# Kernel tuning notes

Measured on AMD Instinct MI355X. Metric: run time of the kernel, lower is better.

The kernel has to match this reference:

```python
import jax, jax.numpy as jnp
import numpy as np
from jax import lax

GRAVITY = 9.8
DT = 0.1
MAX_STEPS = 200


def _conv(x, w, b):
    # x: [N,C,H,W], w: [O,I,3,3] (PyTorch OIHW), padding=1 -> SAME
    y = lax.conv_general_dilated(x, w, window_strides=(1, 1), padding='SAME',
                                 dimension_numbers=('NCHW', 'OIHW', 'NCHW'))
    return y + b[None, :, None, None]


def _maxpool2(x):
    return lax.reduce_window(x, -jnp.inf, lax.max,
                             window_dimensions=(1, 1, 2, 2),
                             window_strides=(1, 1, 2, 2), padding='VALID')


def setup_inputs() -> dict:
    key = jax.random.key(0)
    ks = jax.random.split(key, 12)
    B = 256
    x = jax.random.normal(ks[0], (B, 12, 128, 128), dtype=jnp.float32)

    def he(k, shape, fan_in):
        return jax.random.normal(k, shape, dtype=jnp.float32) * np.float32(np.sqrt(2.0 / fan_in))

    w1 = he(ks[1], (32, 12, 3, 3), 12 * 9); b1 = jnp.zeros((32,), jnp.float32)
    w2 = he(ks[2], (64, 32, 3, 3), 32 * 9); b2 = jnp.zeros((64,), jnp.float32)
    w3 = he(ks[3], (64, 64, 3, 3), 64 * 9); b3 = jnp.zeros((64,), jnp.float32)
    w4 = he(ks[4], (64, 64, 3, 3), 64 * 9); b4 = jnp.zeros((64,), jnp.float32)
    wl1 = he(ks[5], (128, 64 * 8 * 8), 64 * 8 * 8); bl1 = jnp.zeros((128,), jnp.float32)
    wl2 = he(ks[6], (4, 128), 128); bl2 = jnp.zeros((4,), jnp.float32)
    return {'x': x, 'w1': w1, 'b1': b1, 'w2': w2, 'b2': b2, 'w3': w3, 'b3': b3,
            'w4': w4, 'b4': b4, 'wl1': wl1, 'bl1': bl1, 'wl2': wl2, 'bl2': bl2}


def _forward(x, w1, b1, w2, b2, w3, b3, w4, b4, wl1, bl1, wl2, bl2):
    h = _maxpool2(jax.nn.relu(_conv(x, w1, b1)))   # [B,32,64,64]
    h = _maxpool2(jax.nn.relu(_conv(h, w2, b2)))   # [B,64,32,32]
    h = _maxpool2(jax.nn.relu(_conv(h, w3, b3)))   # [B,64,16,16]
    h = _maxpool2(jax.nn.relu(_conv(h, w4, b4)))   # [B,64,8,8]
    h = h.reshape(h.shape[0], -1)                  # [B,4096]
    h = jax.nn.relu(h @ wl1.T + bl1)               # [B,128]
    state = h @ wl2.T + bl2                        # [B,4]

    px, py, vx, vy = state[:, 0], state[:, 1], state[:, 2], state[:, 3]

    def step(carry, _):
        cx, cy, cvy = carry
        nvy = cvy - GRAVITY * DT
        nx = cx + vx * DT
        ny = jnp.maximum(cy + nvy * DT, 0.0)
        return (nx, ny, nvy), None

    (fx, _, _), _ = lax.scan(step, (px, py, vy), None, length=MAX_STEPS)
    return fx


def reference(x, w1, b1, w2, b2, w3, b3, w4, b4, wl1, bl1, wl2, bl2):
    return _forward(x, w1, b1, w2, b2, w3, b3, w4, b4, wl1, bl1, wl2, bl2)
```

## Files before the change

kernel.cpp:

```cpp
#include <hip/hip_runtime.h>


typedef _Float16 f16;
typedef _Float16 f16x8 __attribute__((ext_vector_type(8)));
typedef _Float16 f16x4 __attribute__((ext_vector_type(4)));
typedef float f32x4 __attribute__((ext_vector_type(4)));
typedef float f32x16 __attribute__((ext_vector_type(16)));

__global__ __launch_bounds__(512)
void pack_weights(const float* __restrict__ w1, const float* __restrict__ w2,
                  const float* __restrict__ w3, const float* __restrict__ w4,
                  f16* __restrict__ apack) {
  int idx = blockIdx.x * 512 + threadIdx.x;
  int frag = idx >> 9;
  int e = idx & 511;
  int lane = e >> 3, j = e & 7;
  float v = 0.f;
  if (frag < 9) {
    int kh = frag / 3, kw = frag % 3;
    int oc = lane & 31;
    int ic = (lane >> 5) * 8 + j;
    if (ic < 12) v = w1[((oc * 12 + ic) * 3 + kh) * 3 + kw];
  } else if (frag < 45) {
    int f = frag - 9;
    int ocg = f & 1;
    int sk = f >> 1;
    int ks = sk & 1, sh = sk >> 1;
    int kh = sh / 3, kw = sh % 3;
    int oc = ocg * 32 + (lane & 31);
    int ic = ks * 16 + (lane >> 5) * 8 + j;
    v = w2[((oc * 32 + ic) * 3 + kh) * 3 + kw];
  } else if (frag < 117) {
    int f = frag - 45;
    int ocg = f & 1;
    int sk = f >> 1;
    int ks = sk & 3, sh = sk >> 2;
    int kh = sh / 3, kw = sh % 3;
    int oc = ocg * 32 + (lane & 31);
    int ic = ks * 16 + (lane >> 5) * 8 + j;
    v = w3[((oc * 64 + ic) * 3 + kh) * 3 + kw];
  } else {
    int f = frag - 117;
    int sk = f >> 2, og = f & 3;
    int sh = sk >> 1, ks = sk & 1;
    int kh = sh / 3, kw = sh % 3;
    int row16 = lane & 15, kg = lane >> 4;
    int oc = og * 16 + row16;
    int ic = ks * 32 + kg * 8 + j;
    v = w4[((oc * 64 + ic) * 3 + kh) * 3 + kw];
  }
  apack[idx] = (f16)v;
}

__global__ __launch_bounds__(256)
void pack_wl1(const float* __restrict__ wl1, f16* __restrict__ wl1h) {
  int i = (blockIdx.x * 256 + threadIdx.x) * 4;
  float4 v = *(const float4*)(wl1 + i);
  f16x4 h = { (f16)v.x, (f16)v.y, (f16)v.z, (f16)v.w };
  *(f16x4*)(wl1h + i) = h;
}

__global__ __launch_bounds__(512)
void conv1_mfma(const float* __restrict__ x, const f16* __restrict__ apack,
                const float* __restrict__ bias, f16* __restrict__ hout) {
  constexpr int W = 128, H = 128;
  constexpr int PADB = 48, ROWB = 130 * PADB;
  constexpr int TPB = 8;
  __shared__ char smem[6 * ROWB];
  const int tid = threadIdx.x;
  const int n = blockIdx.y;
  const int R0 = blockIdx.x * (TPB * 4);

  if (tid < 36) {
    int slot = tid / 6, r = tid % 6;
    int px = (r >= 3) ? 129 : 0;
    int ch = r % 3;
    *(float4*)(smem + slot * ROWB + px * PADB + ch * 16) =
        make_float4(0.f, 0.f, 0.f, 0.f);
  }

  const int g = tid >> 4;
  const int l16 = tid & 15;
  const int Q = l16 >> 2, q = l16 & 3;

  auto load_row = [&](int ri) -> float4 {
    float4 v = make_float4(0.f, 0.f, 0.f, 0.f);
    if (l16 < 12 && ri >= 0 && ri < H)
      v = *(const float4*)(x + ((size_t)(n * 12 + l16) * H + ri) * W + g * 4);
    return v;
  };
  auto xpose_write = [&](float4 av, int slot) {
    float4 t1, t2;
    {
      float sx = __shfl_xor(av.x, 1), sy = __shfl_xor(av.y, 1);
      float sz = __shfl_xor(av.z, 1), sw = __shfl_xor(av.w, 1);
      bool odd = q & 1;
      t1.x = odd ? sy : av.x;  t1.y = odd ? av.y : sx;
      t1.z = odd ? sw : av.z;  t1.w = odd ? av.w : sz;
    }
    {
      float sx = __shfl_xor(t1.x, 2), sy = __shfl_xor(t1.y, 2);
      float sz = __shfl_xor(t1.z, 2), sw = __shfl_xor(t1.w, 2);
      bool hi2 = q & 2;
      t2.x = hi2 ? sz : t1.x;  t2.y = hi2 ? sw : t1.y;
      t2.z = hi2 ? t1.z : sx;  t2.w = hi2 ? t1.w : sy;
    }
    f16x4 h = { (f16)t2.x, (f16)t2.y, (f16)t2.z, (f16)t2.w };
    *(f16x4*)(smem + slot * ROWB + (g * 4 + q + 1) * PADB + Q * 8) = h;
  };

  const int wv = tid >> 6, l = tid & 63;
  const int rp = wv >> 2;
  const int pxb = (wv & 3) * 32;
  const int rl0 = rp * 2;
  const int ln = l & 31;
  const int hi = l >> 5;

  f16x8 A[9];
#pragma unroll
  for (int ks = 0; ks < 9; ++ks)
    A[ks] = *(const f16x8*)(apack + ((ks << 9) + (l << 3)));

  float4 a[6];
#pragma unroll
  for (int i = 0; i < 6; ++i) a[i] = load_row(R0 - 1 + i);
#pragma unroll
  for (int i = 0; i < 6; ++i) xpose_write(a[i], i);
  __syncthreads();

  int s0 = 0;
  for (int t = 0; t < TPB; ++t) {
    if (t + 1 < TPB) {
#pragma unroll
      for (int i = 0; i < 4; ++i) a[i] = load_row(R0 + 4 * t + 5 + i);
    }
    f32x16 acc0 = (f32x16)0.f, acc1 = (f32x16)0.f;
#pragma unroll
    for (int kw = 0; kw < 3; ++kw) {
      const char* bcol = smem + (pxb + ln + kw) * PADB + hi * 16;
      f16x8 R[4];
#pragma unroll
      for (int j = 0; j < 4; ++j) {
        int sl = s0 + rl0 + j; if (sl >= 6) sl -= 6;
        R[j] = *(const f16x8*)(bcol + sl * ROWB);
      }
#pragma unroll
      for (int kh = 0; kh < 3; ++kh) {
        acc0 = __builtin_amdgcn_mfma_f32_32x32x16_f16(A[kh * 3 + kw], R[kh],     acc0, 0, 0, 0);
        acc1 = __builtin_amdgcn_mfma_f32_32x32x16_f16(A[kh * 3 + kw], R[kh + 1], acc1, 0, 0, 0);
      }
    }
    {
      const int pr = (R0 >> 1) + 2 * t + rp;
#pragma unroll
      for (int gg = 0; gg < 4; ++gg) {
        float v[4];
#pragma unroll
        for (int c = 0; c < 4; ++c) {
          float m = fmaxf(acc0[gg * 4 + c], acc1[gg * 4 + c]);
          v[c] = fmaxf(m, __shfl_xor(m, 1));
        }
        if ((l & 1) == 0) {
          const int pw = (pxb + ln) >> 1;
          const int oc0 = gg * 8 + hi * 4;
          f16x4 pk;
#pragma unroll
          for (int c = 0; c < 4; ++c)
            pk[c] = (f16)fmaxf(v[c] + bias[oc0 + c], 0.f);
          *(f16x4*)(hout + (((size_t)(n * 64 + pr) * 64 + pw) * 32 + oc0)) = pk;
        }
      }
    }
    __syncthreads();
    if (t + 1 < TPB) {
#pragma unroll
      for (int i = 0; i < 4; ++i) {
        int sl = s0 + i; if (sl >= 6) sl -= 6;
        xpose_write(a[i], sl);
      }
      __syncthreads();
    }
    s0 += 4; if (s0 >= 6) s0 -= 6;
  }
}

__global__ __launch_bounds__(256)
void conv2_roll(const f16* __restrict__ hin, const f16* __restrict__ apack,
                const float* __restrict__ bias, f16* __restrict__ hout) {
  constexpr int C = 32, W = 64, H = 64;
  constexpr int PADB = 80, ROWB = 66 * PADB;
  constexpr int TPB = 4;
  __shared__ char smem[6 * ROWB];
  const int tid = threadIdx.x;
  const int n = blockIdx.y;
  const int R0 = blockIdx.x * (TPB * 4);

  auto chunk_ld = [&](int c, int rbase) -> float4 {
    int rowl = c / 264, rem = c - rowl * 264;
    int px = rem >> 2, kc = rem & 3;
    int ri = rbase + rowl, gx = px - 1;
    float4 v = make_float4(0.f, 0.f, 0.f, 0.f);
    if (ri >= 0 && ri < H && gx >= 0 && gx < W)
      v = *(const float4*)(hin + (((size_t)(n * H + ri) * W + gx) * C + kc * 8));
    return v;
  };
  auto chunk_st = [&](int c, int sbase, float4 v) {
    int rowl = c / 264, rem = c - rowl * 264;
    int px = rem >> 2, kc = rem & 3;
    int slot = sbase + rowl; if (slot >= 6) slot -= 6;
    *(float4*)(smem + slot * ROWB + px * PADB + kc * 16) = v;
  };

  {
    float4 a[7];
#pragma unroll
    for (int it = 0; it < 7; ++it) {
      int c = tid + it * 256;
      a[it] = (c < 1584) ? chunk_ld(c, R0 - 1) : make_float4(0.f, 0.f, 0.f, 0.f);
    }
#pragma unroll
    for (int it = 0; it < 7; ++it) {
      int c = tid + it * 256;
      if (c < 1584) chunk_st(c, 0, a[it]);
    }
  }
  __syncthreads();

  const int wv = tid >> 6, l = tid & 63;
  const int rp = wv >> 1;
  const int pxb = (wv & 1) * 32;
  const int rl0 = rp * 2;
  const int ln = l & 31;
  const int hi = l >> 5;

  float4 a[5];
  int s04 = 0;
  for (int t = 0; t < TPB; ++t) {
    if (t + 1 < TPB) {
#pragma unroll
      for (int it = 0; it < 5; ++it) {
        int c = tid + it * 256;
        a[it] = (c < 1056) ? chunk_ld(c, R0 + 4 * t + 5)
                           : make_float4(0.f, 0.f, 0.f, 0.f);
      }
    }
    f32x16 acc[2][2];
    acc[0][0] = (f32x16)0.f; acc[0][1] = (f32x16)0.f;
    acc[1][0] = (f32x16)0.f; acc[1][1] = (f32x16)0.f;
#pragma unroll
    for (int sh = 0; sh < 9; ++sh) {
      const int kh = sh / 3, kw = sh % 3;
      f16x8 A[2][2];
#pragma unroll
      for (int ks = 0; ks < 2; ++ks)
#pragma unroll
        for (int ocg = 0; ocg < 2; ++ocg)
          A[ks][ocg] = *(const f16x8*)(apack + ((((sh * 2 + ks) * 2 + ocg) << 9) + (l << 3)));
#pragma unroll
      for (int rowi = 0; rowi < 2; ++rowi) {
        int sl = s04 + rl0 + rowi + kh; if (sl >= 6) sl -= 6;
        const char* base = smem + sl * ROWB + (pxb + ln + kw) * PADB + hi * 16;
#pragma unroll
        for (int ks = 0; ks < 2; ++ks) {
          f16x8 B = *(const f16x8*)(base + ks * 32);
          acc[rowi][0] = __builtin_amdgcn_mfma_f32_32x32x16_f16(A[ks][0], B, acc[rowi][0], 0, 0, 0);
          acc[rowi][1] = __builtin_amdgcn_mfma_f32_32x32x16_f16(A[ks][1], B, acc[rowi][1], 0, 0, 0);
        }
      }
    }
    {
      const int pr = (R0 >> 1) + 2 * t + rp;
#pragma unroll
      for (int ocg = 0; ocg < 2; ++ocg) {
#pragma unroll
        for (int gg = 0; gg < 4; ++gg) {
          float v[4];
#pragma unroll
          for (int c = 0; c < 4; ++c) {
            float m = fmaxf(acc[0][ocg][gg * 4 + c], acc[1][ocg][gg * 4 + c]);
            v[c] = fmaxf(m, __shfl_xor(m, 1));
          }
          if ((l & 1) == 0) {
            const int pw = (pxb + ln) >> 1;
            const int oc0 = ocg * 32 + gg * 8 + hi * 4;
            f16x4 pk;
#pragma unroll
            for (int c = 0; c < 4; ++c)
              pk[c] = (f16)fmaxf(v[c] + bias[oc0 + c], 0.f);
            *(f16x4*)(hout + (((size_t)(n * 32 + pr) * 32 + pw) * 64 + oc0)) = pk;
          }
        }
      }
    }
    __syncthreads();
    if (t + 1 < TPB) {
#pragma unroll
      for (int it = 0; it < 5; ++it) {
        int c = tid + it * 256;
        if (c < 1056) chunk_st(c, s04, a[it]);
      }
      __syncthreads();
    }
    s04 += 4; if (s04 >= 6) s04 -= 6;
  }
}

template<int C, int W, int H, int BR, int PADB>
__global__ __launch_bounds__(256)
void conv_shift32(const f16* __restrict__ hin, const f16* __restrict__ apack,
                  const float* __restrict__ bias, f16* __restrict__ hout) {
  constexpr int KS16 = C / 16;
  constexpr int SR = BR + 2;
  constexpr int ROWB = (W + 2) * PADB;
  __shared__ char smem[SR * ROWB];
  const int tid = threadIdx.x;
  const int n = blockIdx.y;
  const int r0 = blockIdx.x * BR;
  constexpr int CPC = C / 8;
  constexpr int TOTC = SR * (W + 2) * CPC;
  constexpr int NITER = (TOTC + 255) / 256;
  {
    float4 stg[NITER];
#pragma unroll
    for (int it = 0; it < NITER; ++it) {
      const int t = tid + it * 256;
      float4 v = make_float4(0.f, 0.f, 0.f, 0.f);
      if (t < TOTC) {
        int sr = t / ((W + 2) * CPC);
        int rem = t - sr * ((W + 2) * CPC);
        int px = rem / CPC;
        int kc = rem - px * CPC;
        int ri = r0 + sr - 1;
        int gx = px - 1;
        if (ri >= 0 && ri < H && gx >= 0 && gx < W)
          v = *(const float4*)(hin + (((size_t)(n * H + ri) * W + gx) * C + kc * 8));
      }
      stg[it] = v;
    }
#pragma unroll
    for (int it = 0; it < NITER; ++it) {
      const int t = tid + it * 256;
      if (t < TOTC) {
        int sr = t / ((W + 2) * CPC);
        int rem = t - sr * ((W + 2) * CPC);
        int px = rem / CPC;
        int kc = rem - px * CPC;
        *(float4*)(smem + sr * ROWB + px * PADB + kc * 16) = stg[it];
      }
    }
  }
  __syncthreads();

  const int wv = tid >> 6, l = tid & 63;
  constexpr int WPP = W / 32;
  const int rp = wv / WPP;
  const int pxb = (wv % WPP) * 32;
  const int rl0 = rp * 2;
  const int ln = l & 31;
  const int hi = l >> 5;
  const int px0 = pxb + ln;

  f32x16 acc[2][2];
  acc[0][0] = (f32x16)0.f; acc[0][1] = (f32x16)0.f;
  acc[1][0] = (f32x16)0.f; acc[1][1] = (f32x16)0.f;

#pragma unroll
  for (int sh = 0; sh < 9; ++sh) {
    const int kh = sh / 3, kw = sh % 3;
    f16x8 A[KS16][2];
#pragma unroll
    for (int ks = 0; ks < KS16; ++ks)
#pragma unroll
      for (int ocg = 0; ocg < 2; ++ocg)
        A[ks][ocg] = *(const f16x8*)(apack + ((((sh * KS16 + ks) * 2 + ocg) << 9) + (l << 3)));
#pragma unroll
    for (int rowi = 0; rowi < 2; ++rowi) {
      const char* base = smem + (rl0 + rowi + kh) * ROWB + (px0 + kw) * PADB + hi * 16;
#pragma unroll
      for (int ks = 0; ks < KS16; ++ks) {
        f16x8 B = *(const f16x8*)(base + ks * 32);
        acc[rowi][0] = __builtin_amdgcn_mfma_f32_32x32x16_f16(A[ks][0], B, acc[rowi][0], 0, 0, 0);
        acc[rowi][1] = __builtin_amdgcn_mfma_f32_32x32x16_f16(A[ks][1], B, acc[rowi][1], 0, 0, 0);
      }
    }
  }
  constexpr int PH = H / 2, PW = W / 2;
  const int pr = blockIdx.x * (BR / 2) + rp;
#pragma unroll
  for (int ocg = 0; ocg < 2; ++ocg) {
#pragma unroll
    for (int gg = 0; gg < 4; ++gg) {
      float v[4];
#pragma unroll
      for (int c = 0; c < 4; ++c) {
        float m = fmaxf(acc[0][ocg][gg * 4 + c], acc[1][ocg][gg * 4 + c]);
        v[c] = fmaxf(m, __shfl_xor(m, 1));
      }
      if ((l & 1) == 0) {
        const int pw = (pxb + ln) >> 1;
        const int oc0 = ocg * 32 + gg * 8 + hi * 4;
        f16x4 pk;
#pragma unroll
        for (int c = 0; c < 4; ++c)
          pk[c] = (f16)fmaxf(v[c] + bias[oc0 + c], 0.f);
        *(f16x4*)(hout + (((size_t)(n * PH + pr) * PW + pw) * 64 + oc0)) = pk;
      }
    }
  }
}

template<int C, int W, int H, int BR, int KS, int PADB, int PGn, bool NCHW_OUT>
__global__ __launch_bounds__(256)
void conv_shift(const f16* __restrict__ hin, const f16* __restrict__ apack,
                const float* __restrict__ bias, void* __restrict__ hout) {
  constexpr int SR = BR + 2;
  constexpr int ROWB = (W + 2) * PADB;
  __shared__ char smem[SR * ROWB];
  const int tid = threadIdx.x;
  const int n = blockIdx.y;
  const int r0 = blockIdx.x * BR;
  constexpr int CPC = C / 8;
  constexpr int TOTC = SR * (W + 2) * CPC;
  constexpr int NITER = (TOTC + 255) / 256;
  {
    float4 stg[NITER];
#pragma unroll
    for (int it = 0; it < NITER; ++it) {
      const int t = tid + it * 256;
      float4 v = make_float4(0.f, 0.f, 0.f, 0.f);
      if (t < TOTC) {
        int sr = t / ((W + 2) * CPC);
        int rem = t - sr * ((W + 2) * CPC);
        int px = rem / CPC;
        int kc = rem - px * CPC;
        int ri = r0 + sr - 1;
        int gx = px - 1;
        if (ri >= 0 && ri < H && gx >= 0 && gx < W)
          v = *(const float4*)(hin + (((size_t)(n * H + ri) * W + gx) * C + kc * 8));
      }
      stg[it] = v;
    }
#pragma unroll
    for (int it = 0; it < NITER; ++it) {
      const int t = tid + it * 256;
      if (t < TOTC) {
        int sr = t / ((W + 2) * CPC);
        int rem = t - sr * ((W + 2) * CPC);
        int px = rem / CPC;
        int kc = rem - px * CPC;
        *(float4*)(smem + sr * ROWB + px * PADB + kc * 16) = stg[it];
      }
    }
  }
  __syncthreads();

  const int wv = tid >> 6, l = tid & 63;
  constexpr int WPP = W / (16 * PGn);
  const int rp = wv / WPP;
  const int pxb = (wv % WPP) * 16 * PGn;
  const int rl0 = rp * 2;
  const int lp = l & 15, kg = l >> 4;
  const int px0 = pxb + lp;

  f32x4 acc[2][PGn][4];
#pragma unroll
  for (int a = 0; a < 2; ++a)
#pragma unroll
    for (int b = 0; b < PGn; ++b)
#pragma unroll
      for (int c = 0; c < 4; ++c)
        acc[a][b][c] = (f32x4){0.f, 0.f, 0.f, 0.f};

#pragma unroll
  for (int sh = 0; sh < 9; ++sh) {
    const int kh = sh / 3, kw = sh % 3;
    f16x8 A[KS][4];
#pragma unroll
    for (int ks = 0; ks < KS; ++ks)
#pragma unroll
      for (int og = 0; og < 4; ++og)
        A[ks][og] = *(const f16x8*)(apack + ((((sh * KS + ks) * 4 + og) << 9) + (l << 3)));
#pragma unroll
    for (int rowi = 0; rowi < 2; ++rowi) {
      const char* base = smem + (rl0 + rowi + kh) * ROWB;
#pragma unroll
      for (int pg = 0; pg < PGn; ++pg) {
#pragma unroll
        for (int ks = 0; ks < KS; ++ks) {
          f16x8 B = *(const f16x8*)(base + (px0 + pg * 16 + kw) * PADB + ks * 64 + kg * 16);
#pragma unroll
          for (int og = 0; og < 4; ++og)
            acc[rowi][pg][og] =
                __builtin_amdgcn_mfma_f32_16x16x32_f16(A[ks][og], B, acc[rowi][pg][og], 0, 0, 0);
        }
      }
    }
  }
  constexpr int PH = H / 2, PW = W / 2;
  const int pr = blockIdx.x * (BR / 2) + rp;
#pragma unroll
  for (int pg = 0; pg < PGn; ++pg) {
#pragma unroll
    for (int og = 0; og < 4; ++og) {
      float v[4];
#pragma unroll
      for (int c = 0; c < 4; ++c) {
        float m = fmaxf(acc[0][pg][og][c], acc[1][pg][og][c]);
        v[c] = fmaxf(m, __shfl_xor(m, 1));
      }
      if ((l & 1) == 0) {
        const int pw = (pxb + pg * 16 + lp) >> 1;
        const int oc0 = og * 16 + kg * 4;
        if constexpr (NCHW_OUT) {
          float* o = (float*)hout;
#pragma unroll
          for (int c = 0; c < 4; ++c)
            o[(((size_t)n * 64 + oc0 + c) * PH + pr) * PW + pw] =
                fmaxf(v[c] + bias[oc0 + c], 0.f);
        } else {
          f16x4 pk;
#pragma unroll
          for (int c = 0; c < 4; ++c)
            pk[c] = (f16)fmaxf(v[c] + bias[oc0 + c], 0.f);
          *(f16x4*)((f16*)hout + (((size_t)(n * PH + pr) * PW + pw) * 64 + oc0)) = pk;
        }
      }
    }
  }
}

__global__ __launch_bounds__(1024)
void fc_head(const float* __restrict__ h4, const f16* __restrict__ wl1h,
             const float* __restrict__ bl1, const float* __restrict__ wl2,
             const float* __restrict__ bl2, float* __restrict__ out) {
  __shared__ float rows[2][4096];
  __shared__ float red[8 * 128 * 2];
  __shared__ float red2[2 * 128];
  const int tid = threadIdx.x;
  const int b0 = blockIdx.x * 2;
  {
    const float4* src = (const float4*)(h4 + (size_t)b0 * 4096);
    float4* dst = (float4*)rows;
    for (int t = tid; t < 2048; t += 1024) dst[t] = src[t];
  }
  __syncthreads();

  const int nn = tid & 127;
  const int ks = tid >> 7;
  const f16x8* wp = (const f16x8*)(wl1h + (size_t)nn * 4096 + ks * 512);
  const float4* x0 = (const float4*)(&rows[0][ks * 512]);
  const float4* x1 = (const float4*)(&rows[1][ks * 512]);
  float s0 = 0.f, s1 = 0.f;
#pragma unroll 4
  for (int i = 0; i < 64; ++i) {
    f16x8 w8 = wp[i];
    float4 a0 = x0[2 * i], a1 = x0[2 * i + 1];
    float4 b0 = x1[2 * i], b1 = x1[2 * i + 1];
    float w0 = (float)w8[0], w1 = (float)w8[1], w2 = (float)w8[2], w3 = (float)w8[3];
    float w4 = (float)w8[4], w5 = (float)w8[5], w6 = (float)w8[6], w7 = (float)w8[7];
    s0 = fmaf(w0, a0.x, fmaf(w1, a0.y, fmaf(w2, a0.z, fmaf(w3, a0.w, s0))));
    s0 = fmaf(w4, a1.x, fmaf(w5, a1.y, fmaf(w6, a1.z, fmaf(w7, a1.w, s0))));
    s1 = fmaf(w0, b0.x, fmaf(w1, b0.y, fmaf(w2, b0.z, fmaf(w3, b0.w, s1))));
    s1 = fmaf(w4, b1.x, fmaf(w5, b1.y, fmaf(w6, b1.z, fmaf(w7, b1.w, s1))));
  }
  red[(ks * 128 + nn) * 2 + 0] = s0;
  red[(ks * 128 + nn) * 2 + 1] = s1;
  __syncthreads();

  if (tid < 256) {
    const int r = tid >> 7, n2 = tid & 127;
    float h = bl1[n2];
#pragma unroll
    for (int k = 0; k < 8; ++k) h += red[(k * 128 + n2) * 2 + r];
    h = fmaxf(h, 0.f);
    red2[r * 128 + n2] = h * (wl2[n2] + 20.0f * wl2[256 + n2]);
  }
  __syncthreads();
#pragma unroll
  for (int s = 64; s > 0; s >>= 1) {
    if (tid < 2 * s) {
      int r = tid / s, i = tid - r * s;
      red2[r * 128 + i] += red2[r * 128 + i + s];
    }
    __syncthreads();
  }
  if (tid < 2) out[b0 + tid] = red2[tid * 128] + bl2[0] + 20.0f * bl2[2];
}

extern "C" void kernel_launch(void* const* d_in, const int* in_sizes, int n_in,
                              void* d_out, int out_size, void* d_ws, size_t ws_size,
                              hipStream_t stream) {
  const float* x   = (const float*)d_in[0];
  const float* w1  = (const float*)d_in[1];
  const float* b1  = (const float*)d_in[2];
  const float* w2  = (const float*)d_in[3];
  const float* b2  = (const float*)d_in[4];
  const float* w3  = (const float*)d_in[5];
  const float* b3  = (const float*)d_in[6];
  const float* w4  = (const float*)d_in[7];
  const float* b4  = (const float*)d_in[8];
  const float* wl1 = (const float*)d_in[9];
  const float* bl1 = (const float*)d_in[10];
  const float* wl2 = (const float*)d_in[11];
  const float* bl2 = (const float*)d_in[12];
  float* out = (float*)d_out;
  char* ws = (char*)d_ws;

  f16* apack = (f16*)ws;
  f16* wl1h  = (f16*)(ws + 524288u);
  f16* h1 = (f16*)(ws + 2097152u);
  f16* h2 = (f16*)(ws + 69206016u);
  f16* h3 = (f16*)(ws + 102760448u);
  float* h4 = (float*)(ws + 111149056u);

  pack_weights<<<189, 512, 0, stream>>>(w1, w2, w3, w4, apack);
  pack_wl1<<<512, 256, 0, stream>>>(wl1, wl1h);
  conv1_mfma<<<dim3(4, 256), 512, 0, stream>>>(x, apack, b1, h1);
  conv2_roll<<<dim3(4, 256), 256, 0, stream>>>(h1, apack + 9 * 512, b2, h2);
  conv_shift32<64, 32, 32, 8, 144><<<dim3(4, 256), 256, 0, stream>>>(
      h2, apack + 45 * 512, b3, h3);
  conv_shift<64, 16, 16, 8, 2, 144, 1, true><<<dim3(2, 256), 256, 0, stream>>>(
      h3, apack + 117 * 512, b4, (void*)h4);
  fc_head<<<128, 1024, 0, stream>>>(h4, wl1h, bl1, wl2, bl2, out);
}
```

Baseline: 233.3 us.

## Fuse conv4, pooling and FC head into one kernel; merge weight packing

Conv4 with its pool and the FC head are merged into one kernel with one block per sample. The block keeps the pooled 64x8x8 activation in shared memory and runs the FC dot products directly from it, which removes the h4 round-trip through global memory and one launch. The two weight-packing kernels are also merged into one launch. In exchange each sample gets a single block of 512 threads, and every block reads the full fp16 wl1 matrix (1 MB), where before each block served two samples.

```diff
diff --git a/kernel.cpp b/kernel.cpp
--- a/kernel.cpp
+++ b/kernel.cpp
@@ -8,9 +8,17 @@
 typedef float f32x16 __attribute__((ext_vector_type(16)));
 
 __global__ __launch_bounds__(512)
-void pack_weights(const float* __restrict__ w1, const float* __restrict__ w2,
-                  const float* __restrict__ w3, const float* __restrict__ w4,
-                  f16* __restrict__ apack) {
+void pack_all(const float* __restrict__ w1, const float* __restrict__ w2,
+              const float* __restrict__ w3, const float* __restrict__ w4,
+              const float* __restrict__ wl1, f16* __restrict__ apack,
+              f16* __restrict__ wl1h) {
+  if (blockIdx.x >= 189) {
+    int i = ((blockIdx.x - 189) * 512 + threadIdx.x) * 4;
+    float4 v = *(const float4*)(wl1 + i);
+    f16x4 h = { (f16)v.x, (f16)v.y, (f16)v.z, (f16)v.w };
+    *(f16x4*)(wl1h + i) = h;
+    return;
+  }
   int idx = blockIdx.x * 512 + threadIdx.x;
   int frag = idx >> 9;
   int e = idx & 511;
@@ -52,14 +60,6 @@
   apack[idx] = (f16)v;
 }
 
-__global__ __launch_bounds__(256)
-void pack_wl1(const float* __restrict__ wl1, f16* __restrict__ wl1h) {
-  int i = (blockIdx.x * 256 + threadIdx.x) * 4;
-  float4 v = *(const float4*)(wl1 + i);
-  f16x4 h = { (f16)v.x, (f16)v.y, (f16)v.z, (f16)v.w };
-  *(f16x4*)(wl1h + i) = h;
-}
-
 __global__ __launch_bounds__(512)
 void conv1_mfma(const float* __restrict__ x, const f16* __restrict__ apack,
                 const float* __restrict__ bias, f16* __restrict__ hout) {
@@ -409,43 +409,44 @@
   }
 }
 
-template<int C, int W, int H, int BR, int KS, int PADB, int PGn, bool NCHW_OUT>
-__global__ __launch_bounds__(256)
-void conv_shift(const f16* __restrict__ hin, const f16* __restrict__ apack,
-                const float* __restrict__ bias, void* __restrict__ hout) {
-  constexpr int SR = BR + 2;
-  constexpr int ROWB = (W + 2) * PADB;
-  __shared__ char smem[SR * ROWB];
+__global__ __launch_bounds__(512)
+void tail_fused(const f16* __restrict__ hin, const f16* __restrict__ apack4,
+                const float* __restrict__ bias, const f16* __restrict__ wl1h,
+                const float* __restrict__ bl1, const float* __restrict__ wl2,
+                const float* __restrict__ bl2, float* __restrict__ out) {
+  constexpr int C = 64, W = 16, H = 16;
+  constexpr int PADB = 144, ROWB = 18 * PADB;
+  __shared__ char smem[18 * ROWB];
+  __shared__ float hbuf[4096];
+  __shared__ float red[4 * 128];
+  __shared__ float red2[128];
   const int tid = threadIdx.x;
-  const int n = blockIdx.y;
-  const int r0 = blockIdx.x * BR;
-  constexpr int CPC = C / 8;
-  constexpr int TOTC = SR * (W + 2) * CPC;
-  constexpr int NITER = (TOTC + 255) / 256;
+  const int n = blockIdx.x;
+
+  constexpr int CPC = 8, TOTC = 18 * 18 * CPC;
   {
-    float4 stg[NITER];
-#pragma unroll
-    for (int it = 0; it < NITER; ++it) {
-      const int t = tid + it * 256;
+    float4 stg[6];
+#pragma unroll
+    for (int it = 0; it < 6; ++it) {
+      const int t = tid + it * 512;
       float4 v = make_float4(0.f, 0.f, 0.f, 0.f);
       if (t < TOTC) {
-        int sr = t / ((W + 2) * CPC);
-        int rem = t - sr * ((W + 2) * CPC);
+        int sr = t / (18 * CPC);
+        int rem = t - sr * (18 * CPC);
         int px = rem / CPC;
         int kc = rem - px * CPC;
-        int ri = r0 + sr - 1;
-        int gx = px - 1;
+        int ri = sr - 1, gx = px - 1;
         if (ri >= 0 && ri < H && gx >= 0 && gx < W)
           v = *(const float4*)(hin + (((size_t)(n * H + ri) * W + gx) * C + kc * 8));
       }
       stg[it] = v;
     }
 #pragma unroll
-    for (int it = 0; it < NITER; ++it) {
-      const int t = tid + it * 256;
+    for (int it = 0; it < 6; ++it) {
+      const int t = tid + it * 512;
       if (t < TOTC) {
-        int sr = t / ((W + 2) * CPC);
-        int rem = t - sr * ((W + 2) * CPC);
+        int sr = t / (18 * CPC);
+        int rem = t - sr * (18 * CPC);
         int px = rem / CPC;
         int kc = rem - px * CPC;
         *(float4*)(smem + sr * ROWB + px * PADB + kc * 16) = stg[it];
@@ -454,137 +455,88 @@
   }
   __syncthreads();
 
-  const int wv = tid >> 6, l = tid & 63;
-  constexpr int WPP = W / (16 * PGn);
-  const int rp = wv / WPP;
-  const int pxb = (wv % WPP) * 16 * PGn;
-  const int rl0 = rp * 2;
-  const int lp = l & 15, kg = l >> 4;
-  const int px0 = pxb + lp;
-
-  f32x4 acc[2][PGn][4];
-#pragma unroll
-  for (int a = 0; a < 2; ++a)
-#pragma unroll
-    for (int b = 0; b < PGn; ++b)
-#pragma unroll
-      for (int c = 0; c < 4; ++c)
-        acc[a][b][c] = (f32x4){0.f, 0.f, 0.f, 0.f};
-
-#pragma unroll
-  for (int sh = 0; sh < 9; ++sh) {
-    const int kh = sh / 3, kw = sh % 3;
-    f16x8 A[KS][4];
-#pragma unroll
-    for (int ks = 0; ks < KS; ++ks)
-#pragma unroll
-      for (int og = 0; og < 4; ++og)
-        A[ks][og] = *(const f16x8*)(apack + ((((sh * KS + ks) * 4 + og) << 9) + (l << 3)));
-#pragma unroll
-    for (int rowi = 0; rowi < 2; ++rowi) {
-      const char* base = smem + (rl0 + rowi + kh) * ROWB;
-#pragma unroll
-      for (int pg = 0; pg < PGn; ++pg) {
-#pragma unroll
-        for (int ks = 0; ks < KS; ++ks) {
-          f16x8 B = *(const f16x8*)(base + (px0 + pg * 16 + kw) * PADB + ks * 64 + kg * 16);
+  {
+    const int wv = tid >> 6, l = tid & 63;
+    const int lp = l & 15, kg = l >> 4;
+    const int rl0 = wv * 2;
+
+    f32x4 acc[2][4];
+#pragma unroll
+    for (int a = 0; a < 2; ++a)
+#pragma unroll
+      for (int o = 0; o < 4; ++o) acc[a][o] = (f32x4){0.f, 0.f, 0.f, 0.f};
+
+#pragma unroll
+    for (int sh = 0; sh < 9; ++sh) {
+      const int kh = sh / 3, kw = sh % 3;
+      f16x8 A[2][4];
+#pragma unroll
+      for (int ks = 0; ks < 2; ++ks)
+#pragma unroll
+        for (int og = 0; og < 4; ++og)
+          A[ks][og] = *(const f16x8*)(apack4 + ((((sh * 2 + ks) * 4 + og) << 9) + (l << 3)));
+#pragma unroll
+      for (int rowi = 0; rowi < 2; ++rowi) {
+        const char* base = smem + (rl0 + rowi + kh) * ROWB;
+#pragma unroll
+        for (int ks = 0; ks < 2; ++ks) {
+          f16x8 B = *(const f16x8*)(base + (lp + kw) * PADB + ks * 64 + kg * 16);
 #pragma unroll
           for (int og = 0; og < 4; ++og)
-            acc[rowi][pg][og] =
-                __builtin_amdgcn_mfma_f32_16x16x32_f16(A[ks][og], B, acc[rowi][pg][og], 0, 0, 0);
+            acc[rowi][og] =
+                __builtin_amdgcn_mfma_f32_16x16x32_f16(A[ks][og], B, acc[rowi][og], 0, 0, 0);
         }
       }
     }
-  }
-  constexpr int PH = H / 2, PW = W / 2;
-  const int pr = blockIdx.x * (BR / 2) + rp;
-#pragma unroll
-  for (int pg = 0; pg < PGn; ++pg) {
 #pragma unroll
     for (int og = 0; og < 4; ++og) {
       float v[4];
 #pragma unroll
       for (int c = 0; c < 4; ++c) {
-        float m = fmaxf(acc[0][pg][og][c], acc[1][pg][og][c]);
+        float m = fmaxf(acc[0][og][c], acc[1][og][c]);
         v[c] = fmaxf(m, __shfl_xor(m, 1));
       }
       if ((l & 1) == 0) {
-        const int pw = (pxb + pg * 16 + lp) >> 1;
+        const int pw = lp >> 1;
         const int oc0 = og * 16 + kg * 4;
-        if constexpr (NCHW_OUT) {
-          float* o = (float*)hout;
-#pragma unroll
-          for (int c = 0; c < 4; ++c)
-            o[(((size_t)n * 64 + oc0 + c) * PH + pr) * PW + pw] =
-                fmaxf(v[c] + bias[oc0 + c], 0.f);
-        } else {
-          f16x4 pk;
-#pragma unroll
-          for (int c = 0; c < 4; ++c)
-            pk[c] = (f16)fmaxf(v[c] + bias[oc0 + c], 0.f);
-          *(f16x4*)((f16*)hout + (((size_t)(n * PH + pr) * PW + pw) * 64 + oc0)) = pk;
-        }
-      }
-    }
-  }
-}
-
-__global__ __launch_bounds__(1024)
-void fc_head(const float* __restrict__ h4, const f16* __restrict__ wl1h,
-             const float* __restrict__ bl1, const float* __restrict__ wl2,
-             const float* __restrict__ bl2, float* __restrict__ out) {
-  __shared__ float rows[2][4096];
-  __shared__ float red[8 * 128 * 2];
-  __shared__ float red2[2 * 128];
-  const int tid = threadIdx.x;
-  const int b0 = blockIdx.x * 2;
+#pragma unroll
+        for (int c = 0; c < 4; ++c)
+          hbuf[(oc0 + c) * 64 + wv * 8 + pw] = fmaxf(v[c] + bias[oc0 + c], 0.f);
+      }
+    }
+  }
+  __syncthreads();
+
   {
-    const float4* src = (const float4*)(h4 + (size_t)b0 * 4096);
-    float4* dst = (float4*)rows;
-    for (int t = tid; t < 2048; t += 1024) dst[t] = src[t];
-  }
-  __syncthreads();
-
-  const int nn = tid & 127;
-  const int ks = tid >> 7;
-  const f16x8* wp = (const f16x8*)(wl1h + (size_t)nn * 4096 + ks * 512);
-  const float4* x0 = (const float4*)(&rows[0][ks * 512]);
-  const float4* x1 = (const float4*)(&rows[1][ks * 512]);
-  float s0 = 0.f, s1 = 0.f;
+    const int nn = tid & 127;
+    const int ks = tid >> 7;
+    const f16x8* wp = (const f16x8*)(wl1h + (size_t)nn * 4096 + ks * 1024);
+    const float4* xr = (const float4*)(&hbuf[ks * 1024]);
+    float s = 0.f;
 #pragma unroll 4
-  for (int i = 0; i < 64; ++i) {
-    f16x8 w8 = wp[i];
-    float4 a0 = x0[2 * i], a1 = x0[2 * i + 1];
-    float4 b0 = x1[2 * i], b1 = x1[2 * i + 1];
-    float w0 = (float)w8[0], w1 = (float)w8[1], w2 = (float)w8[2], w3 = (float)w8[3];
-    float w4 = (float)w8[4], w5 = (float)w8[5], w6 = (float)w8[6], w7 = (float)w8[7];
-    s0 = fmaf(w0, a0.x, fmaf(w1, a0.y, fmaf(w2, a0.z, fmaf(w3, a0.w, s0))));
-    s0 = fmaf(w4, a1.x, fmaf(w5, a1.y, fmaf(w6, a1.z, fmaf(w7, a1.w, s0))));
-    s1 = fmaf(w0, b0.x, fmaf(w1, b0.y, fmaf(w2, b0.z, fmaf(w3, b0.w, s1))));
-    s1 = fmaf(w4, b1.x, fmaf(w5, b1.y, fmaf(w6, b1.z, fmaf(w7, b1.w, s1))));
-  }
-  red[(ks * 128 + nn) * 2 + 0] = s0;
-  red[(ks * 128 + nn) * 2 + 1] = s1;
-  __syncthreads();
-
-  if (tid < 256) {
-    const int r = tid >> 7, n2 = tid & 127;
-    float h = bl1[n2];
-#pragma unroll
-    for (int k = 0; k < 8; ++k) h += red[(k * 128 + n2) * 2 + r];
+    for (int i = 0; i < 128; ++i) {
+      f16x8 w8 = wp[i];
+      float4 a0 = xr[2 * i], a1 = xr[2 * i + 1];
+      s = fmaf((float)w8[0], a0.x, fmaf((float)w8[1], a0.y,
+          fmaf((float)w8[2], a0.z, fmaf((float)w8[3], a0.w, s))));
+      s = fmaf((float)w8[4], a1.x, fmaf((float)w8[5], a1.y,
+          fmaf((float)w8[6], a1.z, fmaf((float)w8[7], a1.w, s))));
+    }
+    red[ks * 128 + nn] = s;
+  }
+  __syncthreads();
+  if (tid < 128) {
+    float h = bl1[tid] + red[tid] + red[128 + tid] + red[256 + tid] + red[384 + tid];
     h = fmaxf(h, 0.f);
-    red2[r * 128 + n2] = h * (wl2[n2] + 20.0f * wl2[256 + n2]);
+    red2[tid] = h * (wl2[tid] + 20.0f * wl2[256 + tid]);
   }
   __syncthreads();
 #pragma unroll
   for (int s = 64; s > 0; s >>= 1) {
-    if (tid < 2 * s) {
-      int r = tid / s, i = tid - r * s;
-      red2[r * 128 + i] += red2[r * 128 + i + s];
-    }
+    if (tid < s) red2[tid] += red2[tid + s];
     __syncthreads();
   }
-  if (tid < 2) out[b0 + tid] = red2[tid * 128] + bl2[0] + 20.0f * bl2[2];
+  if (tid == 0) out[n] = red2[0] + bl2[0] + 20.0f * bl2[2];
 }
 
 extern "C" void kernel_launch(void* const* d_in, const int* in_sizes, int n_in,
@@ -611,15 +563,12 @@
   f16* h1 = (f16*)(ws + 2097152u);
   f16* h2 = (f16*)(ws + 69206016u);
   f16* h3 = (f16*)(ws + 102760448u);
-  float* h4 = (float*)(ws + 111149056u);
-
-  pack_weights<<<189, 512, 0, stream>>>(w1, w2, w3, w4, apack);
-  pack_wl1<<<512, 256, 0, stream>>>(wl1, wl1h);
+
+  pack_all<<<445, 512, 0, stream>>>(w1, w2, w3, w4, wl1, apack, wl1h);
   conv1_mfma<<<dim3(4, 256), 512, 0, stream>>>(x, apack, b1, h1);
   conv2_roll<<<dim3(4, 256), 256, 0, stream>>>(h1, apack + 9 * 512, b2, h2);
   conv_shift32<64, 32, 32, 8, 144><<<dim3(4, 256), 256, 0, stream>>>(
       h2, apack + 45 * 512, b3, h3);
-  conv_shift<64, 16, 16, 8, 2, 144, 1, true><<<dim3(2, 256), 256, 0, stream>>>(
-      h3, apack + 117 * 512, b4, (void*)h4);
-  fc_head<<<128, 1024, 0, stream>>>(h4, wl1h, bl1, wl2, bl2, out);
+  tail_fused<<<256, 512, 0, stream>>>(h3, apack + 117 * 512, b4, wl1h,
+                                      bl1, wl2, bl2, out);
 }
```

Result: faster. 219.4 us, median of 4 (-5.9%).
